# Kernel tuning notes

Hardware: AMD Instinct MI355X
Metric: run time of the kernel (lower is better)

Reference implementation:

```python
import jax, jax.numpy as jnp
import numpy as np

C = 1024
RANK = 8


def _layernorm(x, g, b, eps=1e-5):
    mu = jnp.mean(x, axis=-1, keepdims=True)
    var = jnp.var(x, axis=-1, keepdims=True)
    return (x - mu) * jax.lax.rsqrt(var + eps) * g + b


def setup_inputs() -> dict:
    key = jax.random.key(0)
    ks = jax.random.split(key, 10)
    B, T = 4, 4096
    x = jax.random.normal(ks[0], (B, T, C), dtype=jnp.float32)
    # parameters (match torch inits)
    W0 = jnp.eye(C, dtype=jnp.float32) * 0.1
    A_init = jax.random.normal(ks[1], (C, RANK), dtype=jnp.float32) * 0.01
    B_init = jnp.zeros((RANK, C), dtype=jnp.float32)
    log_lr = jnp.full((C,), float(np.log(0.1)), dtype=jnp.float32)
    s = 1.0 / np.sqrt(C)
    Wq = jax.random.uniform(ks[2], (C, C), minval=-s, maxval=s, dtype=jnp.float32)
    Wk = jax.random.uniform(ks[3], (C, C), minval=-s, maxval=s, dtype=jnp.float32)
    Wv = jax.random.uniform(ks[4], (C, C), minval=-s, maxval=s, dtype=jnp.float32)
    Wo = jax.random.uniform(ks[5], (C, C), minval=-s, maxval=s, dtype=jnp.float32)
    Wg = jax.random.uniform(ks[6], (C, C), minval=-s, maxval=s, dtype=jnp.float32)
    ln_g = jnp.ones((C,), dtype=jnp.float32)
    ln_b = jnp.zeros((C,), dtype=jnp.float32)
    ls_g = jnp.full((C,), 1e-4, dtype=jnp.float32)  # LayerScale gamma
    return {"x": x, "W0": W0, "A_init": A_init, "B_init": B_init,
            "log_lr": log_lr, "Wq": Wq, "Wk": Wk, "Wv": Wv, "Wo": Wo,
            "Wg": Wg, "ln_g": ln_g, "ln_b": ln_b, "ls_g": ls_g}


def reference(x, W0, A_init, B_init, log_lr, Wq, Wk, Wv, Wo, Wg, ln_g, ln_b, ls_g):
    B, T, _ = x.shape
    h = _layernorm(x, ln_g, ln_b)
    # dual-form TTT (training path: q/k/v projections, full K @ W0)
    Q = jnp.einsum('btc,dc->btd', h, Wq)
    K = jnp.einsum('btc,dc->btd', h, Wk)
    V = jnp.einsum('btc,dc->btd', h, Wv)
    lr = jnp.minimum(jnp.exp(log_lr), 1.0)  # clamp(max=1.0)
    y0 = jnp.einsum('btc,cd->btd', K, W0) + jnp.einsum('btr,rd->btd', jnp.einsum('btc,cr->btr', K, A_init), B_init)
    error = y0 - V
    loss = jnp.mean(error ** 2)
    gradient = K * error                     # [B,T,C]
    grad_cumsum = jnp.cumsum(gradient, axis=1)
    grad_shift = jnp.concatenate([jnp.zeros((B, 1, gradient.shape[-1]), gradient.dtype), grad_cumsum[:, :-1, :]], axis=1)
    correction = Q * lr[None, None, :] * grad_shift
    pos = jnp.arange(1, T + 1, dtype=correction.dtype)
    pos_scale = (1.0 / (1.0 + 0.1 * jnp.log(pos)))[None, :, None]
    out = y0 - correction * pos_scale
    # gate, out projection, layer scale, residual
    gate = jax.nn.sigmoid(jnp.einsum('btc,dc->btd', x, Wg))
    out = out * gate
    out = jnp.einsum('btc,dc->btd', out, Wo) * ls_g
    return (x + out, loss)
```

## Files before the change

kernel.cpp:

```cpp
#include <hip/hip_runtime.h>
#include <stdint.h>
#include <math.h>

typedef unsigned short u16;
typedef __attribute__((ext_vector_type(8))) short short8;
typedef __attribute__((ext_vector_type(4))) float f32x4;

__device__ __forceinline__ float bf2f(u16 u){
  union { unsigned int i; float f; } v; v.i = ((unsigned int)u) << 16; return v.f;
}
__device__ __forceinline__ u16 f2bf(float f){
  union { float f; unsigned int i; } v; v.f = f;
  return (u16)((v.i + 0x7FFFu + ((v.i >> 16) & 1u)) >> 16);
}

__global__ void ln_prep(const float* __restrict__ x, const float* __restrict__ g,
                        const float* __restrict__ bta, u16* __restrict__ h,
                        u16* __restrict__ xb, float* __restrict__ loss){
  if (blockIdx.x == 0 && threadIdx.x == 0) loss[0] = 0.f;
  int row = blockIdx.x, tid = threadIdx.x;
  const float4* xr = (const float4*)(x + (size_t)row * 1024);
  float4 v = xr[tid];
  float s  = v.x + v.y + v.z + v.w;
  float s2 = v.x*v.x + v.y*v.y + v.z*v.z + v.w*v.w;
  #pragma unroll
  for (int o = 32; o > 0; o >>= 1){ s += __shfl_down(s, o); s2 += __shfl_down(s2, o); }
  __shared__ float red[8];
  if ((tid & 63) == 0){ red[tid >> 6] = s; red[4 + (tid >> 6)] = s2; }
  __syncthreads();
  float ts = red[0]+red[1]+red[2]+red[3];
  float t2 = red[4]+red[5]+red[6]+red[7];
  float mu   = ts * (1.0f/1024.0f);
  float var  = t2 * (1.0f/1024.0f) - mu*mu;
  float rstd = rsqrtf(var + 1e-5f);
  float4 gg = ((const float4*)g)[tid];
  float4 bb = ((const float4*)bta)[tid];
  ushort4 hv, xv;
  hv.x = f2bf((v.x-mu)*rstd*gg.x + bb.x);
  hv.y = f2bf((v.y-mu)*rstd*gg.y + bb.y);
  hv.z = f2bf((v.z-mu)*rstd*gg.z + bb.z);
  hv.w = f2bf((v.w-mu)*rstd*gg.w + bb.w);
  xv.x = f2bf(v.x); xv.y = f2bf(v.y); xv.z = f2bf(v.z); xv.w = f2bf(v.w);
  ((ushort4*)h )[(size_t)row*256 + tid] = hv;
  ((ushort4*)xb)[(size_t)row*256 + tid] = xv;
}

__global__ void conv5(const float* __restrict__ a, const float* __restrict__ b,
                      const float* __restrict__ c, const float* __restrict__ d,
                      const float* __restrict__ e,
                      u16* oa, u16* ob, u16* oc, u16* od, u16* oe){
  int sel = blockIdx.y;
  const float* s = sel==0?a : sel==1?b : sel==2?c : sel==3?d : e;
  u16* o = sel==0?oa : sel==1?ob : sel==2?oc : sel==3?od : oe;
  int i = blockIdx.x*256 + threadIdx.x;
  float4 v = ((const float4*)s)[i];
  ushort4 r; r.x=f2bf(v.x); r.y=f2bf(v.y); r.z=f2bf(v.z); r.w=f2bf(v.w);
  ((ushort4*)o)[i] = r;
}

__global__ void weff_k(const float* __restrict__ W0, const float* __restrict__ Ai,
                       const float* __restrict__ Bi, u16* __restrict__ Wet){
  __shared__ float tile[32][33];
  int d0 = blockIdx.x*32, e0 = blockIdx.y*32;
  int tid = threadIdx.x;
  int lr = tid >> 5, lc = tid & 31;
  #pragma unroll
  for (int s = 0; s < 4; ++s){
    int e = e0 + s*8 + lr, d = d0 + lc;
    float v = W0[(size_t)e*1024 + d];
    #pragma unroll
    for (int r = 0; r < 8; ++r) v += Ai[e*8 + r] * Bi[(size_t)r*1024 + d];
    tile[s*8 + lr][lc] = v;
  }
  __syncthreads();
  #pragma unroll
  for (int s = 0; s < 4; ++s){
    int d = d0 + s*8 + lr, e = e0 + lc;
    Wet[(size_t)d*1024 + e] = f2bf(tile[lc][s*8 + lr]);
  }
}

#define VMW(N)  asm volatile("s_waitcnt vmcnt(" #N ")" ::: "memory")
#define SBAR    __builtin_amdgcn_s_barrier()
#define SCHED0  __builtin_amdgcn_sched_barrier(0)

template<int EPI>
__device__ __forceinline__ void gemm256_body(const u16* __restrict__ A, const u16* __restrict__ Bm,
    u16* __restrict__ Cb, float* __restrict__ Cf, const float* __restrict__ lsg,
    const float* __restrict__ xres, int mblk, int nblk)
{
  __shared__ u16 As[4][8192];
  __shared__ u16 Bs[4][8192];
  const int tid  = threadIdx.x;
  const int lane = tid & 63;
  const int w    = tid >> 6;
  const int wm = w >> 2, wn = w & 3;
  const int l15 = lane & 15, quad = lane >> 4;
  const int m0 = mblk * 256, n0 = nblk * 256;

  const int sl   = (lane & 7) ^ (lane >> 3);
  const int srow = 2*(w*8 + (lane >> 3)) + (sl >> 2);
  const int scol = (sl & 3) * 8;
  const u16* gA = A  + (size_t)(m0 + srow)*1024 + scol;
  const u16* gB = Bm + (size_t)(n0 + srow)*1024 + scol;
  const int ldsOff = w * 512;

  const int phys8 = (((((l15 & 1) << 2) | quad) ^ (l15 >> 1))) * 8;
  const int rdA = (wm*64 + (l15 >> 1))*64 + phys8;
  const int rdB = (wn*32 + (l15 >> 1))*64 + phys8;

  f32x4 acc[8][4] = {};

#define SA(T) do{ const int _ss=(T)&3; const size_t _k=(size_t)(T)*32; \
    __builtin_amdgcn_global_load_lds((const __attribute__((address_space(1))) unsigned int*)(gA + _k), \
        (__attribute__((address_space(3))) unsigned int*)(&As[_ss][ldsOff]), 16, 0, 0); \
    __builtin_amdgcn_global_load_lds((const __attribute__((address_space(1))) unsigned int*)(gA + _k + 131072), \
        (__attribute__((address_space(3))) unsigned int*)(&As[_ss][ldsOff + 4096]), 16, 0, 0); \
  }while(0)
#define SB(T) do{ const int _ss=(T)&3; const size_t _k=(size_t)(T)*32; \
    __builtin_amdgcn_global_load_lds((const __attribute__((address_space(1))) unsigned int*)(gB + _k), \
        (__attribute__((address_space(3))) unsigned int*)(&Bs[_ss][ldsOff]), 16, 0, 0); \
    __builtin_amdgcn_global_load_lds((const __attribute__((address_space(1))) unsigned int*)(gB + _k + 131072), \
        (__attribute__((address_space(3))) unsigned int*)(&Bs[_ss][ldsOff + 4096]), 16, 0, 0); \
  }while(0)

#define SLICE(T, VMOP, DS) do{ \
    VMOP; \
    SCHED0; SBAR; SCHED0; \
    if (DS){ SA((T)+3); SB((T)+3); } \
    const int _s = (T) & 3; \
    const u16* _as = &As[_s][0]; \
    const u16* _bs = &Bs[_s][0]; \
    short8 afv[8], bfv[4]; \
    _Pragma("unroll") \
    for (int _j = 0; _j < 4; ++_j) bfv[_j] = *(const short8*)(_bs + rdB + _j*512); \
    _Pragma("unroll") \
    for (int _i = 0; _i < 8; ++_i) afv[_i] = *(const short8*)(_as + rdA + _i*512); \
    _Pragma("unroll") \
    for (int _i = 0; _i < 8; ++_i){ \
      _Pragma("unroll") \
      for (int _j = 0; _j < 4; ++_j) \
        acc[_i][_j] = __builtin_amdgcn_mfma_f32_16x16x32_bf16(afv[_i], bfv[_j], acc[_i][_j], 0, 0, 0); \
    } \
  }while(0)

  SA(0); SB(0); SA(1); SB(1); SA(2); SB(2);

  #pragma unroll 1
  for (int t = 0; t < 28; t += 4){
    SLICE(t+0, VMW(8), 1);
    SLICE(t+1, VMW(8), 1);
    SLICE(t+2, VMW(8), 1);
    SLICE(t+3, VMW(8), 1);
  }
  SLICE(28, VMW(8), 1);
  SLICE(29, VMW(8), 0);
  SLICE(30, VMW(4), 0);
  SLICE(31, VMW(0), 0);
#undef SLICE
#undef SA
#undef SB

  const int rbase = quad * 4;
  if (EPI == 0){
    #pragma unroll
    for (int i = 0; i < 8; ++i){
      int row = m0 + wm*128 + i*16 + rbase;
      #pragma unroll
      for (int j = 0; j < 4; ++j){
        int col = n0 + wn*64 + j*16 + l15;
        #pragma unroll
        for (int r = 0; r < 4; ++r)
          Cb[(size_t)(row + r)*1024 + col] = f2bf(acc[i][j][r]);
      }
    }
  } else {
    float lsv[4];
    #pragma unroll
    for (int j = 0; j < 4; ++j) lsv[j] = lsg[n0 + wn*64 + j*16 + l15];
    #pragma unroll
    for (int i = 0; i < 8; ++i){
      int row = m0 + wm*128 + i*16 + rbase;
      #pragma unroll
      for (int j = 0; j < 4; ++j){
        int col = n0 + wn*64 + j*16 + l15;
        #pragma unroll
        for (int r = 0; r < 4; ++r){
          size_t idx = (size_t)(row + r)*1024 + col;
          Cf[idx] = acc[i][j][r] * lsv[j] + xres[idx];
        }
      }
    }
  }
}

__global__ __launch_bounds__(512, 2) void gemm_qkvg(
    const u16* __restrict__ h, const u16* __restrict__ xb,
    const u16* __restrict__ Wqb, const u16* __restrict__ Wkb,
    const u16* __restrict__ Wvb, const u16* __restrict__ Wgb,
    u16* __restrict__ Qb, u16* __restrict__ Kb,
    u16* __restrict__ Vb, u16* __restrict__ Gb){
  int bid = blockIdx.x;
  int swz = (bid & 7) * 128 + (bid >> 3);
  int mblk = swz >> 4;
  int rem  = swz & 15;
  int sel  = rem >> 2, nblk = rem & 3;
  const u16* A  = (sel == 3) ? xb : h;
  const u16* Bm = sel==0?Wqb : sel==1?Wkb : sel==2?Wvb : Wgb;
  u16* Out      = sel==0?Qb  : sel==1?Kb  : sel==2?Vb  : Gb;
  gemm256_body<0>(A, Bm, Out, nullptr, nullptr, nullptr, mblk, nblk);
}

__global__ __launch_bounds__(512, 2) void gemm_plain(
    const u16* __restrict__ A, const u16* __restrict__ Bm, u16* __restrict__ C){
  int bid = blockIdx.x;
  int swz = (bid & 7) * 32 + (bid >> 3);
  gemm256_body<0>(A, Bm, C, nullptr, nullptr, nullptr, swz >> 2, swz & 3);
}

__global__ __launch_bounds__(512, 2) void gemm_final(
    const u16* __restrict__ A, const u16* __restrict__ Bm,
    float* __restrict__ C, const float* __restrict__ lsg,
    const float* __restrict__ xres){
  int bid = blockIdx.x;
  int swz = (bid & 7) * 32 + (bid >> 3);
  gemm256_body<1>(A, Bm, nullptr, C, lsg, xres, swz >> 2, swz & 3);
}

__global__ void scan1(const u16* __restrict__ Kb, const u16* __restrict__ Vb,
                      const u16* __restrict__ Yb, float* __restrict__ part,
                      float* __restrict__ loss){
  int tid = threadIdx.x;
  int c = blockIdx.x*256 + tid;
  int ch = blockIdx.y, b = blockIdx.z;
  size_t base = ((size_t)b*4096 + (size_t)ch*128)*1024 + c;
  float g = 0.f, ls = 0.f;
  #pragma unroll 8
  for (int t = 0; t < 128; ++t){
    size_t idx = base + (size_t)t*1024;
    float kv = bf2f(Kb[idx]), vv = bf2f(Vb[idx]), yv = bf2f(Yb[idx]);
    float e = yv - vv;
    g += kv*e; ls += e*e;
  }
  part[((size_t)(b*32 + ch))*1024 + c] = g;
  #pragma unroll
  for (int o = 32; o > 0; o >>= 1) ls += __shfl_down(ls, o);
  __shared__ float red[4];
  if ((tid & 63) == 0) red[tid >> 6] = ls;
  __syncthreads();
  if (tid == 0) atomicAdd(loss, red[0]+red[1]+red[2]+red[3]);
}

__global__ void scan2(const u16* __restrict__ Kb, const u16* __restrict__ Vb,
                      const u16* __restrict__ Yb, const u16* __restrict__ Qb,
                      const u16* __restrict__ Gb, const float* __restrict__ part,
                      const float* __restrict__ llr, u16* __restrict__ OutPre){
  int tid = threadIdx.x;
  int c = blockIdx.x*256 + tid;
  int ch = blockIdx.y, b = blockIdx.z;
  float run = 0.f;
  for (int j = 0; j < ch; ++j) run += part[((size_t)(b*32 + j))*1024 + c];
  float lrc = fminf(expf(llr[c]), 1.0f);
  size_t base = ((size_t)b*4096 + (size_t)ch*128)*1024 + c;
  #pragma unroll 4
  for (int t = 0; t < 128; ++t){
    size_t idx = base + (size_t)t*1024;
    float kv = bf2f(Kb[idx]), vv = bf2f(Vb[idx]), yv = bf2f(Yb[idx]);
    float qv = bf2f(Qb[idx]), gl = bf2f(Gb[idx]);
    float e = yv - vv;
    int tg = ch*128 + t + 1;
    float ps = 1.0f/(1.0f + 0.1f*logf((float)tg));
    float gate = 1.0f/(1.0f + expf(-gl));
    float o = (yv - qv*lrc*run*ps) * gate;
    OutPre[idx] = f2bf(o);
    run += kv*e;
  }
}

__global__ void finloss(const float* __restrict__ loss, float* __restrict__ o){
  o[0] = loss[0] * (1.0f/16777216.0f);
}

extern "C" void kernel_launch(void* const* d_in, const int* in_sizes, int n_in,
                              void* d_out, int out_size, void* d_ws, size_t ws_size,
                              hipStream_t stream){
  const float* x   = (const float*)d_in[0];
  const float* W0  = (const float*)d_in[1];
  const float* Ai  = (const float*)d_in[2];
  const float* Bi  = (const float*)d_in[3];
  const float* llr = (const float*)d_in[4];
  const float* Wq  = (const float*)d_in[5];
  const float* Wk  = (const float*)d_in[6];
  const float* Wv  = (const float*)d_in[7];
  const float* Wo  = (const float*)d_in[8];
  const float* Wg  = (const float*)d_in[9];
  const float* lng = (const float*)d_in[10];
  const float* lnb = (const float*)d_in[11];
  const float* lsg = (const float*)d_in[12];
  float* out = (float*)d_out;

  const size_t TOK = 16384, CC = 1024;
  char* p = (char*)d_ws;
  float* loss = (float*)p; p += 256;
  u16* h   = (u16*)p; p += TOK*CC*2;
  u16* xb  = (u16*)p; p += TOK*CC*2;
  u16* Qb  = (u16*)p; p += TOK*CC*2;
  u16* Kb  = (u16*)p; p += TOK*CC*2;
  u16* Vb  = (u16*)p; p += TOK*CC*2;
  u16* Gb  = (u16*)p; p += TOK*CC*2;
  u16* Wqb = (u16*)p; p += CC*CC*2;
  u16* Wkb = (u16*)p; p += CC*CC*2;
  u16* Wvb = (u16*)p; p += CC*CC*2;
  u16* Wgb = (u16*)p; p += CC*CC*2;
  u16* Wob = (u16*)p; p += CC*CC*2;
  u16* Wet = (u16*)p; p += CC*CC*2;
  float* part = (float*)p; p += (size_t)4*32*1024*4;

  ln_prep<<<16384, 256, 0, stream>>>(x, lng, lnb, h, xb, loss);
  conv5<<<dim3(1024, 5), 256, 0, stream>>>(Wq, Wk, Wv, Wg, Wo, Wqb, Wkb, Wvb, Wgb, Wob);
  weff_k<<<dim3(32, 32), 256, 0, stream>>>(W0, Ai, Bi, Wet);
  gemm_qkvg<<<1024, 512, 0, stream>>>(h, xb, Wqb, Wkb, Wvb, Wgb, Qb, Kb, Vb, Gb);
  gemm_plain<<<256, 512, 0, stream>>>(Kb, Wet, h);
  scan1<<<dim3(4, 32, 4), 256, 0, stream>>>(Kb, Vb, h, part, loss);
  scan2<<<dim3(4, 32, 4), 256, 0, stream>>>(Kb, Vb, h, Qb, Gb, part, llr, Qb);
  gemm_final<<<256, 512, 0, stream>>>(Qb, Wob, out, lsg, x);
  finloss<<<1, 1, 0, stream>>>(loss, out + 16777216);
}
```

Baseline: 430.7 us.

## Vectorize scans, use one wave per LayerNorm row, and merge small launches

```diff
diff --git a/kernel.cpp b/kernel.cpp
--- a/kernel.cpp
+++ b/kernel.cpp
@@ -17,67 +17,72 @@
 __global__ void ln_prep(const float* __restrict__ x, const float* __restrict__ g,
                         const float* __restrict__ bta, u16* __restrict__ h,
                         u16* __restrict__ xb, float* __restrict__ loss){
-  if (blockIdx.x == 0 && threadIdx.x == 0) loss[0] = 0.f;
-  int row = blockIdx.x, tid = threadIdx.x;
+  int tid = threadIdx.x, wid = tid >> 6, lane = tid & 63;
+  if (blockIdx.x == 0 && tid == 0) loss[0] = 0.f;
+  int row = blockIdx.x * 4 + wid;
   const float4* xr = (const float4*)(x + (size_t)row * 1024);
-  float4 v = xr[tid];
-  float s  = v.x + v.y + v.z + v.w;
-  float s2 = v.x*v.x + v.y*v.y + v.z*v.z + v.w*v.w;
+  float4 v[4]; float s = 0.f, s2 = 0.f;
   #pragma unroll
-  for (int o = 32; o > 0; o >>= 1){ s += __shfl_down(s, o); s2 += __shfl_down(s2, o); }
-  __shared__ float red[8];
-  if ((tid & 63) == 0){ red[tid >> 6] = s; red[4 + (tid >> 6)] = s2; }
-  __syncthreads();
-  float ts = red[0]+red[1]+red[2]+red[3];
-  float t2 = red[4]+red[5]+red[6]+red[7];
-  float mu   = ts * (1.0f/1024.0f);
-  float var  = t2 * (1.0f/1024.0f) - mu*mu;
+  for (int i = 0; i < 4; ++i){
+    v[i] = xr[i*64 + lane];
+    s  += v[i].x + v[i].y + v[i].z + v[i].w;
+    s2 += v[i].x*v[i].x + v[i].y*v[i].y + v[i].z*v[i].z + v[i].w*v[i].w;
+  }
+  #pragma unroll
+  for (int o = 1; o < 64; o <<= 1){ s += __shfl_xor(s, o); s2 += __shfl_xor(s2, o); }
+  float mu   = s * (1.0f/1024.0f);
+  float var  = s2 * (1.0f/1024.0f) - mu*mu;
   float rstd = rsqrtf(var + 1e-5f);
-  float4 gg = ((const float4*)g)[tid];
-  float4 bb = ((const float4*)bta)[tid];
-  ushort4 hv, xv;
-  hv.x = f2bf((v.x-mu)*rstd*gg.x + bb.x);
-  hv.y = f2bf((v.y-mu)*rstd*gg.y + bb.y);
-  hv.z = f2bf((v.z-mu)*rstd*gg.z + bb.z);
-  hv.w = f2bf((v.w-mu)*rstd*gg.w + bb.w);
-  xv.x = f2bf(v.x); xv.y = f2bf(v.y); xv.z = f2bf(v.z); xv.w = f2bf(v.w);
-  ((ushort4*)h )[(size_t)row*256 + tid] = hv;
-  ((ushort4*)xb)[(size_t)row*256 + tid] = xv;
+  #pragma unroll
+  for (int i = 0; i < 4; ++i){
+    float4 gg = ((const float4*)g)[i*64 + lane];
+    float4 bb = ((const float4*)bta)[i*64 + lane];
+    ushort4 hv, xv;
+    hv.x = f2bf((v[i].x-mu)*rstd*gg.x + bb.x);
+    hv.y = f2bf((v[i].y-mu)*rstd*gg.y + bb.y);
+    hv.z = f2bf((v[i].z-mu)*rstd*gg.z + bb.z);
+    hv.w = f2bf((v[i].w-mu)*rstd*gg.w + bb.w);
+    xv.x = f2bf(v[i].x); xv.y = f2bf(v[i].y); xv.z = f2bf(v[i].z); xv.w = f2bf(v[i].w);
+    ((ushort4*)h )[(size_t)row*256 + i*64 + lane] = hv;
+    ((ushort4*)xb)[(size_t)row*256 + i*64 + lane] = xv;
+  }
 }
 
 __global__ void conv5(const float* __restrict__ a, const float* __restrict__ b,
                       const float* __restrict__ c, const float* __restrict__ d,
                       const float* __restrict__ e,
-                      u16* oa, u16* ob, u16* oc, u16* od, u16* oe){
+                      const float* __restrict__ W0, const float* __restrict__ Ai,
+                      const float* __restrict__ Bi,
+                      u16* oa, u16* ob, u16* oc, u16* od, u16* oe,
+                      u16* __restrict__ Wet){
+  __shared__ float tile[32][33];
   int sel = blockIdx.y;
+  int tid = threadIdx.x;
+  if (sel == 5){
+    int d0 = (blockIdx.x & 31)*32, e0 = (blockIdx.x >> 5)*32;
+    int lr = tid >> 5, lc = tid & 31;
+    #pragma unroll
+    for (int s = 0; s < 4; ++s){
+      int ee = e0 + s*8 + lr, dd = d0 + lc;
+      float v = W0[(size_t)ee*1024 + dd];
+      #pragma unroll
+      for (int r = 0; r < 8; ++r) v += Ai[ee*8 + r] * Bi[(size_t)r*1024 + dd];
+      tile[s*8 + lr][lc] = v;
+    }
+    __syncthreads();
+    #pragma unroll
+    for (int s = 0; s < 4; ++s){
+      int dd = d0 + s*8 + lr, ee = e0 + lc;
+      Wet[(size_t)dd*1024 + ee] = f2bf(tile[lc][s*8 + lr]);
+    }
+    return;
+  }
   const float* s = sel==0?a : sel==1?b : sel==2?c : sel==3?d : e;
   u16* o = sel==0?oa : sel==1?ob : sel==2?oc : sel==3?od : oe;
-  int i = blockIdx.x*256 + threadIdx.x;
+  int i = blockIdx.x*256 + tid;
   float4 v = ((const float4*)s)[i];
   ushort4 r; r.x=f2bf(v.x); r.y=f2bf(v.y); r.z=f2bf(v.z); r.w=f2bf(v.w);
   ((ushort4*)o)[i] = r;
-}
-
-__global__ void weff_k(const float* __restrict__ W0, const float* __restrict__ Ai,
-                       const float* __restrict__ Bi, u16* __restrict__ Wet){
-  __shared__ float tile[32][33];
-  int d0 = blockIdx.x*32, e0 = blockIdx.y*32;
-  int tid = threadIdx.x;
-  int lr = tid >> 5, lc = tid & 31;
-  #pragma unroll
-  for (int s = 0; s < 4; ++s){
-    int e = e0 + s*8 + lr, d = d0 + lc;
-    float v = W0[(size_t)e*1024 + d];
-    #pragma unroll
-    for (int r = 0; r < 8; ++r) v += Ai[e*8 + r] * Bi[(size_t)r*1024 + d];
-    tile[s*8 + lr][lc] = v;
-  }
-  __syncthreads();
-  #pragma unroll
-  for (int s = 0; s < 4; ++s){
-    int d = d0 + s*8 + lr, e = e0 + lc;
-    Wet[(size_t)d*1024 + e] = f2bf(tile[lc][s*8 + lr]);
-  }
 }
 
 #define VMW(N)  asm volatile("s_waitcnt vmcnt(" #N ")" ::: "memory")
@@ -221,64 +226,98 @@
 __global__ __launch_bounds__(512, 2) void gemm_final(
     const u16* __restrict__ A, const u16* __restrict__ Bm,
     float* __restrict__ C, const float* __restrict__ lsg,
-    const float* __restrict__ xres){
+    const float* __restrict__ xres, const float* __restrict__ loss){
+  if (blockIdx.x == 0 && threadIdx.x == 0)
+    C[16777216] = loss[0] * (1.0f/16777216.0f);
   int bid = blockIdx.x;
   int swz = (bid & 7) * 32 + (bid >> 3);
   gemm256_body<1>(A, Bm, nullptr, C, lsg, xres, swz >> 2, swz & 3);
 }
 
-__global__ void scan1(const u16* __restrict__ Kb, const u16* __restrict__ Vb,
-                      const u16* __restrict__ Yb, float* __restrict__ part,
-                      float* __restrict__ loss){
+__global__ __launch_bounds__(512) void scan1(
+    const u16* __restrict__ Kb, const u16* __restrict__ Vb,
+    const u16* __restrict__ Yb, float* __restrict__ part,
+    float* __restrict__ loss){
   int tid = threadIdx.x;
-  int c = blockIdx.x*256 + tid;
-  int ch = blockIdx.y, b = blockIdx.z;
-  size_t base = ((size_t)b*4096 + (size_t)ch*128)*1024 + c;
-  float g = 0.f, ls = 0.f;
-  #pragma unroll 8
-  for (int t = 0; t < 128; ++t){
+  int half = tid >> 8;
+  int cq  = tid & 255;
+  int c4  = cq * 4;
+  int ch = blockIdx.x, b = blockIdx.y;
+  size_t base = ((size_t)b*4096 + (size_t)ch*128 + half*64)*1024 + c4;
+  float g0=0.f,g1=0.f,g2=0.f,g3=0.f, ls=0.f;
+  #pragma unroll 4
+  for (int t = 0; t < 64; ++t){
     size_t idx = base + (size_t)t*1024;
-    float kv = bf2f(Kb[idx]), vv = bf2f(Vb[idx]), yv = bf2f(Yb[idx]);
-    float e = yv - vv;
-    g += kv*e; ls += e*e;
-  }
-  part[((size_t)(b*32 + ch))*1024 + c] = g;
+    ushort4 k4 = *(const ushort4*)(Kb + idx);
+    ushort4 v4 = *(const ushort4*)(Vb + idx);
+    ushort4 y4 = *(const ushort4*)(Yb + idx);
+    float e;
+    e = bf2f(y4.x)-bf2f(v4.x); g0 += bf2f(k4.x)*e; ls += e*e;
+    e = bf2f(y4.y)-bf2f(v4.y); g1 += bf2f(k4.y)*e; ls += e*e;
+    e = bf2f(y4.z)-bf2f(v4.z); g2 += bf2f(k4.z)*e; ls += e*e;
+    e = bf2f(y4.w)-bf2f(v4.w); g3 += bf2f(k4.w)*e; ls += e*e;
+  }
+  __shared__ float redg[1024];
+  __shared__ float redl[8];
+  if (half){
+    float4 gv; gv.x=g0; gv.y=g1; gv.z=g2; gv.w=g3;
+    *(float4*)(redg + c4) = gv;
+  }
   #pragma unroll
   for (int o = 32; o > 0; o >>= 1) ls += __shfl_down(ls, o);
-  __shared__ float red[4];
-  if ((tid & 63) == 0) red[tid >> 6] = ls;
+  if ((tid & 63) == 0) redl[tid >> 6] = ls;
   __syncthreads();
-  if (tid == 0) atomicAdd(loss, red[0]+red[1]+red[2]+red[3]);
-}
-
-__global__ void scan2(const u16* __restrict__ Kb, const u16* __restrict__ Vb,
-                      const u16* __restrict__ Yb, const u16* __restrict__ Qb,
-                      const u16* __restrict__ Gb, const float* __restrict__ part,
-                      const float* __restrict__ llr, u16* __restrict__ OutPre){
+  if (!half){
+    float4 gh = *(const float4*)(redg + c4);
+    float4 gv; gv.x=g0+gh.x; gv.y=g1+gh.y; gv.z=g2+gh.z; gv.w=g3+gh.w;
+    *(float4*)(part + (size_t)(b*32 + ch)*1024 + c4) = gv;
+  }
+  if (tid == 0){
+    float L = redl[0]+redl[1]+redl[2]+redl[3]+redl[4]+redl[5]+redl[6]+redl[7];
+    atomicAdd(loss, L);
+  }
+}
+
+__global__ __launch_bounds__(256) void scan2(
+    const u16* __restrict__ Kb, const u16* __restrict__ Vb,
+    const u16* __restrict__ Yb, const u16* __restrict__ Qb,
+    const u16* __restrict__ Gb, const float* __restrict__ part,
+    const float* __restrict__ llr, u16* __restrict__ OutPre){
   int tid = threadIdx.x;
-  int c = blockIdx.x*256 + tid;
-  int ch = blockIdx.y, b = blockIdx.z;
-  float run = 0.f;
-  for (int j = 0; j < ch; ++j) run += part[((size_t)(b*32 + j))*1024 + c];
-  float lrc = fminf(expf(llr[c]), 1.0f);
-  size_t base = ((size_t)b*4096 + (size_t)ch*128)*1024 + c;
+  int c4 = tid * 4;
+  int ch = blockIdx.x, b = blockIdx.y;
+  float r0=0.f,r1=0.f,r2=0.f,r3=0.f;
+  for (int j = 0; j < ch; ++j){
+    float4 p = *(const float4*)(part + (size_t)(b*32 + j)*1024 + c4);
+    r0 += p.x; r1 += p.y; r2 += p.z; r3 += p.w;
+  }
+  float4 ll = *(const float4*)(llr + c4);
+  float lr0 = fminf(__expf(ll.x), 1.0f);
+  float lr1 = fminf(__expf(ll.y), 1.0f);
+  float lr2 = fminf(__expf(ll.z), 1.0f);
+  float lr3 = fminf(__expf(ll.w), 1.0f);
+  size_t base = ((size_t)b*4096 + (size_t)ch*128)*1024 + c4;
   #pragma unroll 4
   for (int t = 0; t < 128; ++t){
     size_t idx = base + (size_t)t*1024;
-    float kv = bf2f(Kb[idx]), vv = bf2f(Vb[idx]), yv = bf2f(Yb[idx]);
-    float qv = bf2f(Qb[idx]), gl = bf2f(Gb[idx]);
-    float e = yv - vv;
-    int tg = ch*128 + t + 1;
-    float ps = 1.0f/(1.0f + 0.1f*logf((float)tg));
-    float gate = 1.0f/(1.0f + expf(-gl));
-    float o = (yv - qv*lrc*run*ps) * gate;
-    OutPre[idx] = f2bf(o);
-    run += kv*e;
-  }
-}
-
-__global__ void finloss(const float* __restrict__ loss, float* __restrict__ o){
-  o[0] = loss[0] * (1.0f/16777216.0f);
+    ushort4 k4 = *(const ushort4*)(Kb + idx);
+    ushort4 v4 = *(const ushort4*)(Vb + idx);
+    ushort4 y4 = *(const ushort4*)(Yb + idx);
+    ushort4 q4 = *(const ushort4*)(Qb + idx);
+    ushort4 g4 = *(const ushort4*)(Gb + idx);
+    float ps = 1.0f/(1.0f + 0.1f*__logf((float)(ch*128 + t + 1)));
+    ushort4 ov;
+    float e, gate, o;
+    e = bf2f(y4.x)-bf2f(v4.x); gate = 1.0f/(1.0f + __expf(-bf2f(g4.x)));
+    o = (bf2f(y4.x) - bf2f(q4.x)*lr0*r0*ps) * gate; ov.x = f2bf(o); r0 += bf2f(k4.x)*e;
+    e = bf2f(y4.y)-bf2f(v4.y); gate = 1.0f/(1.0f + __expf(-bf2f(g4.y)));
+    o = (bf2f(y4.y) - bf2f(q4.y)*lr1*r1*ps) * gate; ov.y = f2bf(o); r1 += bf2f(k4.y)*e;
+    e = bf2f(y4.z)-bf2f(v4.z); gate = 1.0f/(1.0f + __expf(-bf2f(g4.z)));
+    o = (bf2f(y4.z) - bf2f(q4.z)*lr2*r2*ps) * gate; ov.z = f2bf(o); r2 += bf2f(k4.z)*e;
+    e = bf2f(y4.w)-bf2f(v4.w); gate = 1.0f/(1.0f + __expf(-bf2f(g4.w)));
+    o = (bf2f(y4.w) - bf2f(q4.w)*lr3*r3*ps) * gate; ov.w = f2bf(o); r3 += bf2f(k4.w)*e;
+    *(ushort4*)(OutPre + idx) = ov;
+  }
 }
 
 extern "C" void kernel_launch(void* const* d_in, const int* in_sizes, int n_in,
@@ -316,13 +355,12 @@
   u16* Wet = (u16*)p; p += CC*CC*2;
   float* part = (float*)p; p += (size_t)4*32*1024*4;
 
-  ln_prep<<<16384, 256, 0, stream>>>(x, lng, lnb, h, xb, loss);
-  conv5<<<dim3(1024, 5), 256, 0, stream>>>(Wq, Wk, Wv, Wg, Wo, Wqb, Wkb, Wvb, Wgb, Wob);
-  weff_k<<<dim3(32, 32), 256, 0, stream>>>(W0, Ai, Bi, Wet);
+  ln_prep<<<4096, 256, 0, stream>>>(x, lng, lnb, h, xb, loss);
+  conv5<<<dim3(1024, 6), 256, 0, stream>>>(Wq, Wk, Wv, Wg, Wo, W0, Ai, Bi,
+                                           Wqb, Wkb, Wvb, Wgb, Wob, Wet);
   gemm_qkvg<<<1024, 512, 0, stream>>>(h, xb, Wqb, Wkb, Wvb, Wgb, Qb, Kb, Vb, Gb);
   gemm_plain<<<256, 512, 0, stream>>>(Kb, Wet, h);
-  scan1<<<dim3(4, 32, 4), 256, 0, stream>>>(Kb, Vb, h, part, loss);
-  scan2<<<dim3(4, 32, 4), 256, 0, stream>>>(Kb, Vb, h, Qb, Gb, part, llr, Qb);
-  gemm_final<<<256, 512, 0, stream>>>(Qb, Wob, out, lsg, x);
-  finloss<<<1, 1, 0, stream>>>(loss, out + 16777216);
-}
+  scan1<<<dim3(32, 4), 512, 0, stream>>>(Kb, Vb, h, part, loss);
+  scan2<<<dim3(32, 4), 256, 0, stream>>>(Kb, Vb, h, Qb, Gb, part, llr, Qb);
+  gemm_final<<<256, 512, 0, stream>>>(Qb, Wob, out, lsg, x, loss);
+}
```

Measured after the change: 505.5 us. 17.4% more time.
